# Performance work log

Measured on AMD Instinct MI355X. Metric: run time of the kernel, lower is better.

## Reference

```python
import jax, jax.numpy as jnp
import numpy as np

TOP_K = 2
NUM_EXPERTS = 64
LOAD_BALANCE_ALPHA = 0.01
Z_LOSS_ALPHA = 1e-4
TEMPERATURE = 1.0  # buffer init, clamped to [0.1, 2.0] -> 1.0 (seq_len < 8192 branch)


def setup_inputs() -> dict:
    key = jax.random.key(0)
    k1, k2 = jax.random.split(key)
    x = jax.random.normal(k1, (4, 4096, 1024), dtype=jnp.float32)
    gate_w = jax.random.normal(k2, (NUM_EXPERTS, 1024), dtype=jnp.float32) * (1.0 / np.sqrt(1024))
    return {"x": x, "gate_w": gate_w}


def reference(x, gate_w):
    B, S, H = x.shape
    x_flat = x.reshape(-1, H)                      # [T, H], T = B*S
    logits = jnp.einsum('th,eh->te', x_flat, gate_w)  # [T, E]
    logits = logits / TEMPERATURE
    scores = jax.nn.softmax(logits, axis=-1)       # [T, E]
    # eval path: dynamic_top_k == top_k, no noise / capacity limitation
    top_scores, top_idx = jax.lax.top_k(scores, TOP_K)   # [T, K]
    top_scores = jax.nn.softmax(top_scores.astype(jnp.float32), axis=-1).astype(x.dtype)
    # load-balance loss: squared deviation of mean expert load from uniform
    expert_load = scores.mean(axis=0)              # [E]
    ideal = 1.0 / NUM_EXPERTS
    lb_loss = LOAD_BALANCE_ALPHA * NUM_EXPERTS * jnp.sum((expert_load - ideal) ** 2)
    # z-loss: mean squared logsumexp of gate logits
    z = jax.nn.logsumexp(logits, axis=-1)          # [T]
    z_loss = Z_LOSS_ALPHA * jnp.mean(z ** 2)
    total_loss = lb_loss + z_loss
    return top_scores, top_idx, total_loss
```

## Files before the change

kernel.cpp:

```cpp
#include <hip/hip_runtime.h>
#include <math.h>

#define T_TOK 16384
#define NEXP  64


__global__ void moe_prep(const float* __restrict__ gw, float* __restrict__ ws) {
    __shared__ float tile[64][65];
    const int b = blockIdx.x;
    const int tid = threadIdx.x;
    if (b == 0 && tid < 128) ws[tid] = 0.f;
#pragma unroll
    for (int it = 0; it < 16; ++it) {
        int idx = it * 256 + tid;
        int e = idx >> 6, kk = idx & 63;
        tile[e][kk] = gw[e * 1024 + b * 64 + kk];
    }
    __syncthreads();
#pragma unroll
    for (int it = 0; it < 16; ++it) {
        int idx = it * 256 + tid;
        int kk = idx >> 6, e = idx & 63;
        ws[128 + (b * 64 + kk) * 64 + e] = tile[e][kk];
    }
}

__launch_bounds__(512, 2)
__global__ void moe_main(const float* __restrict__ x,
                         const float* __restrict__ wt,
                         float* __restrict__ acc_ws,
                         float* __restrict__ out) {
    __shared__ float xbuf[2][4096];
    __shared__ float sc[64][65];
    __shared__ float row_inv[64];
    __shared__ float colpart[8][64];
    __shared__ int   is_last;

    const int tid  = threadIdx.x;
    const int lane = tid & 63;
    const int wv   = tid >> 6;
    const int g = __builtin_amdgcn_readfirstlane(wv & 3);
    const int h = __builtin_amdgcn_readfirstlane(wv >> 2);
    const int tok0 = blockIdx.x << 6;

    const int tile = wv >> 2;
    const int rr0  = ((wv & 3) << 4) + (lane >> 4);
    const int cg   = lane & 15;
    const float* gbase = x + (((size_t)(tok0 + rr0)) << 10) + (tile << 9) + (cg << 2);
    const int lo0 = (tile << 12) + ((rr0 +  0) << 6) + ((cg ^ ((rr0 +  0) & 15)) << 2);
    const int lo1 = (tile << 12) + ((rr0 +  4) << 6) + ((cg ^ ((rr0 +  4) & 15)) << 2);
    const int lo2 = (tile << 12) + ((rr0 +  8) << 6) + ((cg ^ ((rr0 +  8) & 15)) << 2);
    const int lo3 = (tile << 12) + ((rr0 + 12) << 6) + ((cg ^ ((rr0 + 12) & 15)) << 2);
    float* xb = &xbuf[0][0];

    float acc[16];
#pragma unroll
    for (int e = 0; e < 16; ++e) acc[e] = 0.f;

    float4 p0 = *(const float4*)(gbase);
    float4 p1 = *(const float4*)(gbase + 4096);
    float4 p2 = *(const float4*)(gbase + 8192);
    float4 p3 = *(const float4*)(gbase + 12288);

    const int swz = cg;
    const float* xrow = &xbuf[h][lane << 6];

#pragma unroll 1
    for (int s = 0; s < 8; ++s) {
        __syncthreads();
        *(float4*)(xb + lo0) = p0;
        *(float4*)(xb + lo1) = p1;
        *(float4*)(xb + lo2) = p2;
        *(float4*)(xb + lo3) = p3;
        __syncthreads();
        if (s < 7) {
            const float* gs = gbase + ((s + 1) << 6);
            p0 = *(const float4*)(gs);
            p1 = *(const float4*)(gs + 4096);
            p2 = *(const float4*)(gs + 8192);
            p3 = *(const float4*)(gs + 12288);
        }
        const float* wrow = wt + (((h << 9) + (s << 6)) << 6) + (g << 4);
#pragma unroll
        for (int c = 0; c < 16; ++c) {
            float4 xv = *(const float4*)(xrow + ((c ^ swz) << 2));
            float xa[4] = {xv.x, xv.y, xv.z, xv.w};
#pragma unroll
            for (int j = 0; j < 4; ++j) {
                const float* wkj = wrow + (((c << 2) + j) << 6);
                float xj = xa[j];
#pragma unroll
                for (int e = 0; e < 16; ++e)
                    acc[e] = fmaf(xj, wkj[e], acc[e]);
            }
        }
    }

    if (h == 0) {
#pragma unroll
        for (int e = 0; e < 16; ++e) sc[lane][(g << 4) + e] = acc[e];
    }
    __syncthreads();
    if (h == 1) {
#pragma unroll
        for (int e = 0; e < 16; ++e) sc[lane][(g << 4) + e] += acc[e];
    }
    __syncthreads();

    if (tid < 64) {
        const int r = tid;
        float v1 = -1e30f, v2 = -1e30f;
        int i1 = 0, i2 = 0;
        for (int j = 0; j < 64; ++j) {
            float l = sc[r][j];
            if (l > v1)      { v2 = v1; i2 = i1; v1 = l; i1 = j; }
            else if (l > v2) { v2 = l; i2 = j; }
        }
        float m = v1;
        float ssum = 0.f;
        for (int j = 0; j < 64; ++j) {
            float ev = expf(sc[r][j] - m);
            ssum += ev;
            sc[r][j] = ev;
        }
        float inv = 1.f / ssum;
        row_inv[r] = inv;
        float z = m + logf(ssum);
        float zsq = z * z;
#pragma unroll
        for (int off = 32; off > 0; off >>= 1) zsq += __shfl_down(zsq, off);
        if (lane == 0) atomicAdd(acc_ws + 64, zsq);

        float p1s = inv;
        float p2s = expf(v2 - m) * inv;
        float bb  = expf(p2s - p1s);
        float s1 = 1.f / (1.f + bb);
        float s2 = bb * s1;
        int t = tok0 + r;
        out[2 * t]     = s1;
        out[2 * t + 1] = s2;
        out[2 * T_TOK + 2 * t]     = (float)i1;
        out[2 * T_TOK + 2 * t + 1] = (float)i2;
    }
    __syncthreads();

    {
        int e  = tid & 63;
        int rg = tid >> 6;
        float sum = 0.f;
#pragma unroll
        for (int r2 = 0; r2 < 8; ++r2) {
            int row = (rg << 3) + r2;
            sum += sc[row][e] * row_inv[row];
        }
        colpart[rg][e] = sum;
    }
    __syncthreads();
    if (tid < 64) {
        float tot = 0.f;
#pragma unroll
        for (int rg = 0; rg < 8; ++rg) tot += colpart[rg][tid];
        atomicAdd(acc_ws + tid, tot);
    }

    __syncthreads();
    if (tid == 0) {
        __threadfence();
        int old = __hip_atomic_fetch_add((int*)(acc_ws + 66), 1,
                                         __ATOMIC_ACQ_REL, __HIP_MEMORY_SCOPE_AGENT);
        is_last = (old == 255) ? 1 : 0;
    }
    __syncthreads();
    if (is_last && tid < 64) {
        __threadfence();
        float load = __hip_atomic_load(acc_ws + tid, __ATOMIC_RELAXED,
                                       __HIP_MEMORY_SCOPE_AGENT) * (1.f / 16384.f);
        float d = load - (1.f / 64.f);
        float v = d * d;
#pragma unroll
        for (int off = 32; off > 0; off >>= 1) v += __shfl_down(v, off);
        if (tid == 0) {
            float zsum = __hip_atomic_load(acc_ws + 64, __ATOMIC_RELAXED,
                                           __HIP_MEMORY_SCOPE_AGENT);
            float lb = 0.01f * 64.f * v;
            float zl = 1e-4f * zsum * (1.f / 16384.f);
            out[4 * T_TOK] = lb + zl;
        }
    }
}

extern "C" void kernel_launch(void* const* d_in, const int* in_sizes, int n_in,
                              void* d_out, int out_size, void* d_ws, size_t ws_size,
                              hipStream_t stream) {
    const float* x  = (const float*)d_in[0];
    const float* gw = (const float*)d_in[1];
    float* out = (float*)d_out;
    float* ws  = (float*)d_ws;

    moe_prep<<<16, 256, 0, stream>>>(gw, ws);
    moe_main<<<256, 512, 0, stream>>>(x, ws + 128, ws, out);
}
```

Before: 146.0 us.

## Double threads per block and split each K-chunk across four wave groups

```diff
diff --git a/kernel.cpp b/kernel.cpp
--- a/kernel.cpp
+++ b/kernel.cpp
@@ -25,7 +25,7 @@
     }
 }
 
-__launch_bounds__(512, 2)
+__launch_bounds__(1024, 4)
 __global__ void moe_main(const float* __restrict__ x,
                          const float* __restrict__ wt,
                          float* __restrict__ acc_ws,
@@ -33,24 +33,22 @@
     __shared__ float xbuf[2][4096];
     __shared__ float sc[64][65];
     __shared__ float row_inv[64];
-    __shared__ float colpart[8][64];
+    __shared__ float colpart[16][64];
     __shared__ int   is_last;
 
     const int tid  = threadIdx.x;
     const int lane = tid & 63;
     const int wv   = tid >> 6;
-    const int g = __builtin_amdgcn_readfirstlane(wv & 3);
-    const int h = __builtin_amdgcn_readfirstlane(wv >> 2);
+    const int g     = __builtin_amdgcn_readfirstlane(wv & 3);
+    const int h     = __builtin_amdgcn_readfirstlane(wv >> 2);
+    const int khalf = __builtin_amdgcn_readfirstlane(h >> 1);
+    const int cq    = __builtin_amdgcn_readfirstlane(h & 1);
     const int tok0 = blockIdx.x << 6;
 
-    const int tile = wv >> 2;
-    const int rr0  = ((wv & 3) << 4) + (lane >> 4);
-    const int cg   = lane & 15;
-    const float* gbase = x + (((size_t)(tok0 + rr0)) << 10) + (tile << 9) + (cg << 2);
-    const int lo0 = (tile << 12) + ((rr0 +  0) << 6) + ((cg ^ ((rr0 +  0) & 15)) << 2);
-    const int lo1 = (tile << 12) + ((rr0 +  4) << 6) + ((cg ^ ((rr0 +  4) & 15)) << 2);
-    const int lo2 = (tile << 12) + ((rr0 +  8) << 6) + ((cg ^ ((rr0 +  8) & 15)) << 2);
-    const int lo3 = (tile << 12) + ((rr0 + 12) << 6) + ((cg ^ ((rr0 + 12) & 15)) << 2);
+    const int rr = tid >> 4;
+    const int cg = tid & 15;
+    const float* gbase = x + (((size_t)(tok0 + rr)) << 10) + (cg << 2);
+    const int lo = (rr << 6) + ((cg ^ (rr & 15)) << 2);
     float* xb = &xbuf[0][0];
 
     float acc[16];
@@ -58,36 +56,31 @@
     for (int e = 0; e < 16; ++e) acc[e] = 0.f;
 
     float4 p0 = *(const float4*)(gbase);
-    float4 p1 = *(const float4*)(gbase + 4096);
-    float4 p2 = *(const float4*)(gbase + 8192);
-    float4 p3 = *(const float4*)(gbase + 12288);
-
-    const int swz = cg;
-    const float* xrow = &xbuf[h][lane << 6];
+    float4 p1 = *(const float4*)(gbase + 512);
+
+    const int swz = lane & 15;
+    const float* xrow = &xbuf[khalf][lane << 6];
 
 #pragma unroll 1
     for (int s = 0; s < 8; ++s) {
         __syncthreads();
-        *(float4*)(xb + lo0) = p0;
-        *(float4*)(xb + lo1) = p1;
-        *(float4*)(xb + lo2) = p2;
-        *(float4*)(xb + lo3) = p3;
+        *(float4*)(xb + lo)        = p0;
+        *(float4*)(xb + lo + 4096) = p1;
         __syncthreads();
         if (s < 7) {
             const float* gs = gbase + ((s + 1) << 6);
             p0 = *(const float4*)(gs);
-            p1 = *(const float4*)(gs + 4096);
-            p2 = *(const float4*)(gs + 8192);
-            p3 = *(const float4*)(gs + 12288);
-        }
-        const float* wrow = wt + (((h << 9) + (s << 6)) << 6) + (g << 4);
-#pragma unroll
-        for (int c = 0; c < 16; ++c) {
-            float4 xv = *(const float4*)(xrow + ((c ^ swz) << 2));
+            p1 = *(const float4*)(gs + 512);
+        }
+        const float* wrow = wt + (((khalf << 9) + (s << 6)) << 6) + (g << 4);
+#pragma unroll
+        for (int c = 0; c < 8; ++c) {
+            int cc = (cq << 3) + c;
+            float4 xv = *(const float4*)(xrow + ((cc ^ swz) << 2));
             float xa[4] = {xv.x, xv.y, xv.z, xv.w};
 #pragma unroll
             for (int j = 0; j < 4; ++j) {
-                const float* wkj = wrow + (((c << 2) + j) << 6);
+                const float* wkj = wrow + (((cc << 2) + j) << 6);
                 float xj = xa[j];
 #pragma unroll
                 for (int e = 0; e < 16; ++e)
@@ -102,6 +95,16 @@
     }
     __syncthreads();
     if (h == 1) {
+#pragma unroll
+        for (int e = 0; e < 16; ++e) sc[lane][(g << 4) + e] += acc[e];
+    }
+    __syncthreads();
+    if (h == 2) {
+#pragma unroll
+        for (int e = 0; e < 16; ++e) sc[lane][(g << 4) + e] += acc[e];
+    }
+    __syncthreads();
+    if (h == 3) {
 #pragma unroll
         for (int e = 0; e < 16; ++e) sc[lane][(g << 4) + e] += acc[e];
     }
@@ -149,8 +152,8 @@
         int rg = tid >> 6;
         float sum = 0.f;
 #pragma unroll
-        for (int r2 = 0; r2 < 8; ++r2) {
-            int row = (rg << 3) + r2;
+        for (int r2 = 0; r2 < 4; ++r2) {
+            int row = (rg << 2) + r2;
             sum += sc[row][e] * row_inv[row];
         }
         colpart[rg][e] = sum;
@@ -159,7 +162,7 @@
     if (tid < 64) {
         float tot = 0.f;
 #pragma unroll
-        for (int rg = 0; rg < 8; ++rg) tot += colpart[rg][tid];
+        for (int rg = 0; rg < 16; ++rg) tot += colpart[rg][tid];
         atomicAdd(acc_ws + tid, tot);
     }
 
@@ -198,5 +201,5 @@
     float* ws  = (float*)d_ws;
 
     moe_prep<<<16, 256, 0, stream>>>(gw, ws);
-    moe_main<<<256, 512, 0, stream>>>(x, ws + 128, ws, out);
+    moe_main<<<256, 1024, 0, stream>>>(x, ws + 128, ws, out);
 }
```

Measured after the change: 134.8 us. -7.7%, faster.
